# Kernel optimization log

Measured on AMD Instinct MI355X. Metric: run time of the kernel, lower is better.

Reference implementation:

```python
import jax, jax.numpy as jnp
import numpy as np

B = 16384          # batch
WIDTH = 128        # nodes per DAG layer
N_HIDDEN = 30      # hidden layers
DEG = 16           # in-degree of each non-source node
N_WL = N_HIDDEN + 1            # weighted layers (hidden + sink layer) = 31
N_NODES = (N_WL + 1) * WIDTH   # 32 layers * 128 = 4096 total DAG nodes


def setup_inputs() -> dict:
    rng = np.random.default_rng(0)
    # Mask M per layer: (preds+bias, layer_width); bias row (last) is all ones.
    masks = np.zeros((N_WL, WIDTH + 1, WIDTH), np.float32)
    masks[:, -1, :] = 1.0
    for l in range(N_WL):
        for j in range(WIDTH):
            rows = rng.choice(WIDTH, size=DEG, replace=False)
            masks[l, rows, j] = 1.0
    # kaiming_uniform_(a=sqrt(5)) on (nnz,1) tensors has fan_in=1 -> U(-1,1) per nnz entry.
    weights = (rng.uniform(-1.0, 1.0, masks.shape).astype(np.float32)) * masks
    # Layered DAG: preds of weighted layer l are exactly the nodes of layer l (global ids l*W..(l+1)*W).
    preds_idx = np.stack([np.arange(l * WIDTH, (l + 1) * WIDTH) for l in range(N_WL)]).astype(np.int32)
    layers_idx = preds_idx + WIDTH  # nodes written by weighted layer l
    x = jax.random.normal(jax.random.key(0), (B, WIDTH), jnp.float32)
    return {
        "x": x,
        "weights": jnp.asarray(weights),
        "masks": jnp.asarray(masks),
        "preds_idx": jnp.asarray(preds_idx),
        "layers_idx": jnp.asarray(layers_idx),
    }


def reference(x, weights, masks, preds_idx, layers_idx):
    b = x.shape[0]
    act = jnp.zeros((b, N_NODES), x.dtype)
    act = act.at[:, :WIDTH].set(x)           # activations[:, sources] = x
    ones = jnp.ones((b, 1), x.dtype)         # bias column (bias=True)
    # dropout p=0.0 -> identity

    def step(act, layer_inputs):
        W, M, preds, layer = layer_inputs
        h = jnp.concatenate([jnp.take(act, preds, axis=1), ones], axis=1)  # [b, preds+1]
        out = jax.nn.relu(h @ (M * W))                                     # [b, width]
        return act.at[:, layer].set(out), None

    act, _ = jax.lax.scan(step, act, (weights, masks, preds_idx, layers_idx))
    sinks = layers_idx[-1]
    return jnp.take(act, sinks, axis=1)       # activations[:, sinks]
```

## Files before the change

### kernel.cpp

```cpp
#include <hip/hip_runtime.h>
#include <stdint.h>

#define NWL 31

typedef __attribute__((ext_vector_type(8))) short short8;
typedef __attribute__((ext_vector_type(4))) float f32x4;
typedef __attribute__((ext_vector_type(4))) uint32_t u32x4;

#define WCOMP 32768
#define WLAYER 65536
#define WS_W_BYTES (NWL * WLAYER)

#define LDS_WBUF0 0
#define LDS_WBUF1 65536
#define LDS_ACT   131072
#define LDS_TOTAL 163840

__device__ __forceinline__ uint16_t f2bf(float f) {
  uint32_t u = __builtin_bit_cast(uint32_t, f);
  u += 0x7FFFu + ((u >> 16) & 1u);
  return (uint16_t)(u >> 16);
}
__device__ __forceinline__ float bf2f(uint16_t b) {
  return __builtin_bit_cast(float, (uint32_t)b << 16);
}

__device__ __forceinline__ uint32_t perm_hihi(uint32_t hi, uint32_t lo) {
#if __has_builtin(__builtin_amdgcn_perm)
  return __builtin_amdgcn_perm(hi, lo, 0x07060302u);
#else
  return (hi & 0xFFFF0000u) | (lo >> 16);
#endif
}
__device__ __forceinline__ uint32_t perm_lolo(uint32_t hi, uint32_t lo) {
#if __has_builtin(__builtin_amdgcn_perm)
  return __builtin_amdgcn_perm(hi, lo, 0x05040100u);
#else
  return (hi << 16) | (lo & 0xFFFFu);
#endif
}

__device__ __forceinline__ void gload_lds16(const void* g, void* l) {
  __builtin_amdgcn_global_load_lds(
      (const __attribute__((address_space(1))) uint32_t*)g,
      (__attribute__((address_space(3))) uint32_t*)l, 16, 0, 0);
}

__global__ __launch_bounds__(512)
void prep_weights(const float* __restrict__ W, const float* __restrict__ M,
                  char* __restrict__ wsW, float* __restrict__ wsB) {
  const int l    = blockIdx.x >> 2;
  const int kk   = blockIdx.x & 3;
  const int nt   = threadIdx.x >> 6;
  const int lane = threadIdx.x & 63;
  const int kbase = kk * 32 + ((lane >> 4) << 3);
  const int n     = (nt << 4) + (lane & 15);
  const float* Wl = W + l * 129 * 128;
  const float* Ml = M + l * 129 * 128;
  short8 vh, vl;
#pragma unroll
  for (int i = 0; i < 8; ++i) {
    const int k = kbase + i;
    const float v = Wl[k * 128 + n] * Ml[k * 128 + n];
    const uint16_t h = f2bf(v);
    vh[i] = (short)h;
    vl[i] = (short)f2bf(v - bf2f(h));
  }
  char* base = wsW + l * WLAYER;
  const int frag = ((kk * 8 + nt) * 64 + lane) * 16;
  *(short8*)(base + frag)         = vh;
  *(short8*)(base + WCOMP + frag) = vl;
  if (kk == 0 && threadIdx.x < 128) {
    const int t = threadIdx.x;
    wsB[l * 128 + t] = Wl[128 * 128 + t] * Ml[128 * 128 + t];
  }
}

__global__ __launch_bounds__(512, 2)
void dag_mlp(const float* __restrict__ x, const char* __restrict__ wsW,
             const float* __restrict__ wsB, float* __restrict__ out) {
  extern __shared__ char lds[];
  const int tid  = threadIdx.x;
  const int lane = tid & 63;
  const int wv   = tid >> 6;
  const int wm   = wv >> 2;
  const int wn   = wv & 3;
  const int l16  = lane & 15;
  const int g4   = lane >> 4;
  const int r0   = blockIdx.x << 6;

#pragma unroll
  for (int r = 0; r < 8; ++r) {
    const int off = r * 8192 + wv * 1024;
    gload_lds16(wsW + off + lane * 16, lds + LDS_WBUF0 + off);
  }

#pragma unroll
  for (int it = 0; it < 4; ++it) {
    const int idx = tid + it * 512;
    const int row = idx >> 5;
    const int cq  = idx & 31;
    const f32x4 v = *(const f32x4*)(x + (size_t)(r0 + row) * 128 + cq * 4);
    u32x4 w;
#pragma unroll
    for (int c = 0; c < 4; ++c) {
      const uint32_t u  = __builtin_bit_cast(uint32_t, v[c]);
      const float    hi = __builtin_bit_cast(float, u & 0xFFFF0000u);
      const uint32_t ur = __builtin_bit_cast(uint32_t, v[c] - hi);
      w[c] = perm_hihi(ur, u);
    }
    const int off = row * 512 + ((cq ^ (row & 7)) << 4);
    *(u32x4*)(lds + LDS_ACT + off) = w;
  }

  int aoff[2][4][2];
#pragma unroll
  for (int fr = 0; fr < 2; ++fr) {
    const int arow = wm * 32 + fr * 16 + l16;
#pragma unroll
    for (int kk = 0; kk < 4; ++kk) {
      const int g0 = kk * 8 + g4 * 2;
      aoff[fr][kk][0] = arow * 512 + (((g0    ) ^ (arow & 7)) << 4);
      aoff[fr][kk][1] = arow * 512 + (((g0 + 1) ^ (arow & 7)) << 4);
    }
  }
  int boff[4][2];
#pragma unroll
  for (int kk = 0; kk < 4; ++kk)
#pragma unroll
    for (int fc = 0; fc < 2; ++fc)
      boff[kk][fc] = (((kk * 8 + wn * 2 + fc) * 64 + lane) << 4);
  int eoff[2][2][4];
#pragma unroll
  for (int fr = 0; fr < 2; ++fr)
#pragma unroll
    for (int fc = 0; fc < 2; ++fc) {
      const int col = wn * 32 + fc * 16 + l16;
#pragma unroll
      for (int i = 0; i < 4; ++i) {
        const int row = wm * 32 + fr * 16 + g4 * 4 + i;
        eoff[fr][fc][i] = row * 512 + (((col >> 2) ^ (row & 7)) << 4) + ((col & 3) << 2);
      }
    }
  const float* biasp = wsB + wn * 32 + l16;

  __syncthreads();

  int wsel = 0;
  for (int l = 0; l < NWL; ++l) {
    if (l + 1 < NWL) {
      const char* g = wsW + (size_t)(l + 1) * WLAYER;
      const int dst = wsel ^ 65536;
#pragma unroll
      for (int r = 0; r < 8; ++r) {
        const int off = r * 8192 + wv * 1024;
        gload_lds16(g + off + lane * 16, lds + dst + off);
      }
    }
    const float bias0 = biasp[l * 128];
    const float bias1 = biasp[l * 128 + 16];

    u32x4 ah[2][4], al[2][4];
#pragma unroll
    for (int fr = 0; fr < 2; ++fr)
#pragma unroll
      for (int kk = 0; kk < 4; ++kk) {
        const u32x4 p0 = *(const u32x4*)(lds + LDS_ACT + aoff[fr][kk][0]);
        const u32x4 p1 = *(const u32x4*)(lds + LDS_ACT + aoff[fr][kk][1]);
        ah[fr][kk][0] = perm_lolo(p0[1], p0[0]);
        ah[fr][kk][1] = perm_lolo(p0[3], p0[2]);
        ah[fr][kk][2] = perm_lolo(p1[1], p1[0]);
        ah[fr][kk][3] = perm_lolo(p1[3], p1[2]);
        al[fr][kk][0] = perm_hihi(p0[1], p0[0]);
        al[fr][kk][1] = perm_hihi(p0[3], p0[2]);
        al[fr][kk][2] = perm_hihi(p1[1], p1[0]);
        al[fr][kk][3] = perm_hihi(p1[3], p1[2]);
      }

    f32x4 acc[2][2];
#pragma unroll
    for (int fr = 0; fr < 2; ++fr)
#pragma unroll
      for (int fc = 0; fc < 2; ++fc) {
        f32x4 z = {0.f, 0.f, 0.f, 0.f};
        acc[fr][fc] = z;
      }

#pragma unroll
    for (int kk = 0; kk < 4; ++kk) {
      short8 bH[2], bL[2];
#pragma unroll
      for (int fc = 0; fc < 2; ++fc) {
        const char* p = lds + wsel + boff[kk][fc];
        bH[fc] = *(const short8*)(p);
        bL[fc] = *(const short8*)(p + WCOMP);
      }
#pragma unroll
      for (int fr = 0; fr < 2; ++fr) {
        const short8 aH = __builtin_bit_cast(short8, ah[fr][kk]);
#pragma unroll
        for (int fc = 0; fc < 2; ++fc)
          acc[fr][fc] = __builtin_amdgcn_mfma_f32_16x16x32_bf16(aH, bH[fc], acc[fr][fc], 0, 0, 0);
      }
#pragma unroll
      for (int fr = 0; fr < 2; ++fr) {
        const short8 aL = __builtin_bit_cast(short8, al[fr][kk]);
#pragma unroll
        for (int fc = 0; fc < 2; ++fc)
          acc[fr][fc] = __builtin_amdgcn_mfma_f32_16x16x32_bf16(aL, bH[fc], acc[fr][fc], 0, 0, 0);
      }
#pragma unroll
      for (int fr = 0; fr < 2; ++fr) {
        const short8 aH = __builtin_bit_cast(short8, ah[fr][kk]);
#pragma unroll
        for (int fc = 0; fc < 2; ++fc)
          acc[fr][fc] = __builtin_amdgcn_mfma_f32_16x16x32_bf16(aH, bL[fc], acc[fr][fc], 0, 0, 0);
      }
    }

    __syncthreads();

    if (l == NWL - 1) {
#pragma unroll
      for (int fr = 0; fr < 2; ++fr)
#pragma unroll
        for (int fc = 0; fc < 2; ++fc) {
          const float bias = fc ? bias1 : bias0;
          const int col = wn * 32 + fc * 16 + l16;
#pragma unroll
          for (int i = 0; i < 4; ++i) {
            const int row = r0 + wm * 32 + fr * 16 + g4 * 4 + i;
            out[(size_t)row * 128 + col] = fmaxf(acc[fr][fc][i] + bias, 0.0f);
          }
        }
    } else {
#pragma unroll
      for (int fr = 0; fr < 2; ++fr)
#pragma unroll
        for (int fc = 0; fc < 2; ++fc) {
          const float bias = fc ? bias1 : bias0;
#pragma unroll
          for (int i = 0; i < 4; ++i) {
            const float v = fmaxf(acc[fr][fc][i] + bias, 0.0f);
            const uint32_t u  = __builtin_bit_cast(uint32_t, v);
            const float    hi = __builtin_bit_cast(float, u & 0xFFFF0000u);
            const uint32_t ur = __builtin_bit_cast(uint32_t, v - hi);
            *(uint32_t*)(lds + LDS_ACT + eoff[fr][fc][i]) = perm_hihi(ur, u);
          }
        }
      __syncthreads();
      wsel ^= 65536;
    }
  }
}

extern "C" void kernel_launch(void* const* d_in, const int* in_sizes, int n_in,
                              void* d_out, int out_size, void* d_ws, size_t ws_size,
                              hipStream_t stream) {
  const float* x = (const float*)d_in[0];
  const float* W = (const float*)d_in[1];
  const float* M = (const float*)d_in[2];
  char*  wsW = (char*)d_ws;
  float* wsB = (float*)((char*)d_ws + WS_W_BYTES);
  float* out = (float*)d_out;

  (void)hipFuncSetAttribute((const void*)dag_mlp,
                            hipFuncAttributeMaxDynamicSharedMemorySize, LDS_TOTAL);

  hipLaunchKernelGGL(prep_weights, dim3(NWL * 4), dim3(512), 0, stream, W, M, wsW, wsB);
  hipLaunchKernelGGL(dag_mlp, dim3(256), dim3(512), LDS_TOTAL, stream, x, wsW, wsB, out);
}
```

Measured before the change: 130.2 us.

## Load weight fragments directly into registers and double-buffer activations in LDS

Weight fragments are no longer staged through LDS with global_load_lds. Each wave now loads its own B fragments for the next layer straight from global memory (L2) into a register double buffer (B0/B1). Activations ping-pong between two LDS buffers, which leaves one barrier per layer instead of two and cuts LDS use from 160KB to 64KB. In exchange, register pressure goes up by 128 VGPRs for the weight buffers, and every wave refetches weights from global memory or cache instead of sharing one LDS copy.

```diff
diff --git a/kernel.cpp b/kernel.cpp
--- a/kernel.cpp
+++ b/kernel.cpp
@@ -11,10 +11,9 @@
 #define WLAYER 65536
 #define WS_W_BYTES (NWL * WLAYER)
 
-#define LDS_WBUF0 0
-#define LDS_WBUF1 65536
-#define LDS_ACT   131072
-#define LDS_TOTAL 163840
+#define LDS_ACT0 0
+#define LDS_ACT1 32768
+#define LDS_TOTAL 65536
 
 __device__ __forceinline__ uint16_t f2bf(float f) {
   uint32_t u = __builtin_bit_cast(uint32_t, f);
@@ -38,12 +37,6 @@
 #else
   return (hi << 16) | (lo & 0xFFFFu);
 #endif
-}
-
-__device__ __forceinline__ void gload_lds16(const void* g, void* l) {
-  __builtin_amdgcn_global_load_lds(
-      (const __attribute__((address_space(1))) uint32_t*)g,
-      (__attribute__((address_space(3))) uint32_t*)l, 16, 0, 0);
 }
 
 __global__ __launch_bounds__(512)
@@ -90,12 +83,6 @@
   const int r0   = blockIdx.x << 6;
 
 #pragma unroll
-  for (int r = 0; r < 8; ++r) {
-    const int off = r * 8192 + wv * 1024;
-    gload_lds16(wsW + off + lane * 16, lds + LDS_WBUF0 + off);
-  }
-
-#pragma unroll
   for (int it = 0; it < 4; ++it) {
     const int idx = tid + it * 512;
     const int row = idx >> 5;
@@ -110,7 +97,7 @@
       w[c] = perm_hihi(ur, u);
     }
     const int off = row * 512 + ((cq ^ (row & 7)) << 4);
-    *(u32x4*)(lds + LDS_ACT + off) = w;
+    *(u32x4*)(lds + LDS_ACT0 + off) = w;
   }
 
   int aoff[2][4][2];
@@ -124,12 +111,6 @@
       aoff[fr][kk][1] = arow * 512 + (((g0 + 1) ^ (arow & 7)) << 4);
     }
   }
-  int boff[4][2];
-#pragma unroll
-  for (int kk = 0; kk < 4; ++kk)
-#pragma unroll
-    for (int fc = 0; fc < 2; ++fc)
-      boff[kk][fc] = (((kk * 8 + wn * 2 + fc) * 64 + lane) << 4);
   int eoff[2][2][4];
 #pragma unroll
   for (int fr = 0; fr < 2; ++fr)
@@ -142,116 +123,109 @@
         eoff[fr][fc][i] = row * 512 + (((col >> 2) ^ (row & 7)) << 4) + ((col & 3) << 2);
       }
     }
-  const float* biasp = wsB + wn * 32 + l16;
+  const float* biasL = wsB + wn * 32 + l16;
+  const char*  wlane = wsW + wn * 2048 + (size_t)lane * 16;
+
+  u32x4 B0[16], B1[16];
+#pragma unroll
+  for (int kk = 0; kk < 4; ++kk)
+#pragma unroll
+    for (int fc = 0; fc < 2; ++fc)
+#pragma unroll
+      for (int hl = 0; hl < 2; ++hl)
+        B0[kk * 4 + fc * 2 + hl] =
+            *(const u32x4*)(wlane + kk * 8192 + fc * 1024 + hl * 32768);
 
   __syncthreads();
 
-  int wsel = 0;
-  for (int l = 0; l < NWL; ++l) {
-    if (l + 1 < NWL) {
-      const char* g = wsW + (size_t)(l + 1) * WLAYER;
-      const int dst = wsel ^ 65536;
-#pragma unroll
-      for (int r = 0; r < 8; ++r) {
-        const int off = r * 8192 + wv * 1024;
-        gload_lds16(g + off + lane * 16, lds + dst + off);
-      }
-    }
-    const float bias0 = biasp[l * 128];
-    const float bias1 = biasp[l * 128 + 16];
-
-    u32x4 ah[2][4], al[2][4];
-#pragma unroll
-    for (int fr = 0; fr < 2; ++fr)
-#pragma unroll
-      for (int kk = 0; kk < 4; ++kk) {
-        const u32x4 p0 = *(const u32x4*)(lds + LDS_ACT + aoff[fr][kk][0]);
-        const u32x4 p1 = *(const u32x4*)(lds + LDS_ACT + aoff[fr][kk][1]);
-        ah[fr][kk][0] = perm_lolo(p0[1], p0[0]);
-        ah[fr][kk][1] = perm_lolo(p0[3], p0[2]);
-        ah[fr][kk][2] = perm_lolo(p1[1], p1[0]);
-        ah[fr][kk][3] = perm_lolo(p1[3], p1[2]);
-        al[fr][kk][0] = perm_hihi(p0[1], p0[0]);
-        al[fr][kk][1] = perm_hihi(p0[3], p0[2]);
-        al[fr][kk][2] = perm_hihi(p1[1], p1[0]);
-        al[fr][kk][3] = perm_hihi(p1[3], p1[2]);
-      }
-
-    f32x4 acc[2][2];
-#pragma unroll
-    for (int fr = 0; fr < 2; ++fr)
-#pragma unroll
-      for (int fc = 0; fc < 2; ++fc) {
-        f32x4 z = {0.f, 0.f, 0.f, 0.f};
-        acc[fr][fc] = z;
-      }
-
-#pragma unroll
-    for (int kk = 0; kk < 4; ++kk) {
-      short8 bH[2], bL[2];
-#pragma unroll
-      for (int fc = 0; fc < 2; ++fc) {
-        const char* p = lds + wsel + boff[kk][fc];
-        bH[fc] = *(const short8*)(p);
-        bL[fc] = *(const short8*)(p + WCOMP);
-      }
-#pragma unroll
-      for (int fr = 0; fr < 2; ++fr) {
-        const short8 aH = __builtin_bit_cast(short8, ah[fr][kk]);
-#pragma unroll
-        for (int fc = 0; fc < 2; ++fc)
-          acc[fr][fc] = __builtin_amdgcn_mfma_f32_16x16x32_bf16(aH, bH[fc], acc[fr][fc], 0, 0, 0);
-      }
-#pragma unroll
-      for (int fr = 0; fr < 2; ++fr) {
-        const short8 aL = __builtin_bit_cast(short8, al[fr][kk]);
-#pragma unroll
-        for (int fc = 0; fc < 2; ++fc)
-          acc[fr][fc] = __builtin_amdgcn_mfma_f32_16x16x32_bf16(aL, bH[fc], acc[fr][fc], 0, 0, 0);
-      }
-#pragma unroll
-      for (int fr = 0; fr < 2; ++fr) {
-        const short8 aH = __builtin_bit_cast(short8, ah[fr][kk]);
-#pragma unroll
-        for (int fc = 0; fc < 2; ++fc)
-          acc[fr][fc] = __builtin_amdgcn_mfma_f32_16x16x32_bf16(aH, bL[fc], acc[fr][fc], 0, 0, 0);
-      }
-    }
-
-    __syncthreads();
-
-    if (l == NWL - 1) {
-#pragma unroll
-      for (int fr = 0; fr < 2; ++fr)
-#pragma unroll
-        for (int fc = 0; fc < 2; ++fc) {
-          const float bias = fc ? bias1 : bias0;
-          const int col = wn * 32 + fc * 16 + l16;
-#pragma unroll
-          for (int i = 0; i < 4; ++i) {
-            const int row = r0 + wm * 32 + fr * 16 + g4 * 4 + i;
-            out[(size_t)row * 128 + col] = fmaxf(acc[fr][fc][i] + bias, 0.0f);
-          }
-        }
-    } else {
-#pragma unroll
-      for (int fr = 0; fr < 2; ++fr)
-#pragma unroll
-        for (int fc = 0; fc < 2; ++fc) {
-          const float bias = fc ? bias1 : bias0;
-#pragma unroll
-          for (int i = 0; i < 4; ++i) {
-            const float v = fmaxf(acc[fr][fc][i] + bias, 0.0f);
-            const uint32_t u  = __builtin_bit_cast(uint32_t, v);
-            const float    hi = __builtin_bit_cast(float, u & 0xFFFF0000u);
-            const uint32_t ur = __builtin_bit_cast(uint32_t, v - hi);
-            *(uint32_t*)(lds + LDS_ACT + eoff[fr][fc][i]) = perm_hihi(ur, u);
-          }
-        }
-      __syncthreads();
-      wsel ^= 65536;
-    }
-  }
+#define LAYER_BODY(l, Bc, Bn, RDB, WRB, LAST, PREF)                            \
+  do {                                                                         \
+    if (PREF) {                                                                \
+      const char* wl = wlane + (size_t)((l) + 1) * WLAYER;                     \
+      _Pragma("unroll") for (int kk = 0; kk < 4; ++kk)                         \
+      _Pragma("unroll") for (int fc = 0; fc < 2; ++fc)                         \
+      _Pragma("unroll") for (int hl = 0; hl < 2; ++hl)                         \
+        (Bn)[kk * 4 + fc * 2 + hl] =                                           \
+            *(const u32x4*)(wl + kk * 8192 + fc * 1024 + hl * 32768);          \
+    }                                                                          \
+    const float bias0 = biasL[(l) * 128];                                      \
+    const float bias1 = biasL[(l) * 128 + 16];                                 \
+    f32x4 acc[2][2];                                                           \
+    _Pragma("unroll") for (int fr = 0; fr < 2; ++fr)                           \
+    _Pragma("unroll") for (int fc = 0; fc < 2; ++fc) {                         \
+      f32x4 z = {0.f, 0.f, 0.f, 0.f};                                          \
+      acc[fr][fc] = z;                                                         \
+    }                                                                          \
+    _Pragma("unroll") for (int kk = 0; kk < 4; ++kk) {                         \
+      const u32x4 p00 = *(const u32x4*)(lds + (RDB) + aoff[0][kk][0]);         \
+      const u32x4 p01 = *(const u32x4*)(lds + (RDB) + aoff[0][kk][1]);         \
+      const u32x4 p10 = *(const u32x4*)(lds + (RDB) + aoff[1][kk][0]);         \
+      const u32x4 p11 = *(const u32x4*)(lds + (RDB) + aoff[1][kk][1]);         \
+      u32x4 h0, l0, h1, l1;                                                    \
+      h0[0] = perm_lolo(p00[1], p00[0]);  h0[1] = perm_lolo(p00[3], p00[2]);   \
+      h0[2] = perm_lolo(p01[1], p01[0]);  h0[3] = perm_lolo(p01[3], p01[2]);   \
+      l0[0] = perm_hihi(p00[1], p00[0]);  l0[1] = perm_hihi(p00[3], p00[2]);   \
+      l0[2] = perm_hihi(p01[1], p01[0]);  l0[3] = perm_hihi(p01[3], p01[2]);   \
+      h1[0] = perm_lolo(p10[1], p10[0]);  h1[1] = perm_lolo(p10[3], p10[2]);   \
+      h1[2] = perm_lolo(p11[1], p11[0]);  h1[3] = perm_lolo(p11[3], p11[2]);   \
+      l1[0] = perm_hihi(p10[1], p10[0]);  l1[1] = perm_hihi(p10[3], p10[2]);   \
+      l1[2] = perm_hihi(p11[1], p11[0]);  l1[3] = perm_hihi(p11[3], p11[2]);   \
+      const short8 a0H = __builtin_bit_cast(short8, h0);                       \
+      const short8 a0L = __builtin_bit_cast(short8, l0);                       \
+      const short8 a1H = __builtin_bit_cast(short8, h1);                       \
+      const short8 a1L = __builtin_bit_cast(short8, l1);                       \
+      const short8 bH0 = __builtin_bit_cast(short8, (Bc)[kk * 4 + 0]);         \
+      const short8 bL0 = __builtin_bit_cast(short8, (Bc)[kk * 4 + 1]);         \
+      const short8 bH1 = __builtin_bit_cast(short8, (Bc)[kk * 4 + 2]);         \
+      const short8 bL1 = __builtin_bit_cast(short8, (Bc)[kk * 4 + 3]);         \
+      acc[0][0] = __builtin_amdgcn_mfma_f32_16x16x32_bf16(a0H, bH0, acc[0][0], 0, 0, 0); \
+      acc[0][1] = __builtin_amdgcn_mfma_f32_16x16x32_bf16(a0H, bH1, acc[0][1], 0, 0, 0); \
+      acc[1][0] = __builtin_amdgcn_mfma_f32_16x16x32_bf16(a1H, bH0, acc[1][0], 0, 0, 0); \
+      acc[1][1] = __builtin_amdgcn_mfma_f32_16x16x32_bf16(a1H, bH1, acc[1][1], 0, 0, 0); \
+      acc[0][0] = __builtin_amdgcn_mfma_f32_16x16x32_bf16(a0L, bH0, acc[0][0], 0, 0, 0); \
+      acc[0][1] = __builtin_amdgcn_mfma_f32_16x16x32_bf16(a0L, bH1, acc[0][1], 0, 0, 0); \
+      acc[1][0] = __builtin_amdgcn_mfma_f32_16x16x32_bf16(a1L, bH0, acc[1][0], 0, 0, 0); \
+      acc[1][1] = __builtin_amdgcn_mfma_f32_16x16x32_bf16(a1L, bH1, acc[1][1], 0, 0, 0); \
+      acc[0][0] = __builtin_amdgcn_mfma_f32_16x16x32_bf16(a0H, bL0, acc[0][0], 0, 0, 0); \
+      acc[0][1] = __builtin_amdgcn_mfma_f32_16x16x32_bf16(a0H, bL1, acc[0][1], 0, 0, 0); \
+      acc[1][0] = __builtin_amdgcn_mfma_f32_16x16x32_bf16(a1H, bL0, acc[1][0], 0, 0, 0); \
+      acc[1][1] = __builtin_amdgcn_mfma_f32_16x16x32_bf16(a1H, bL1, acc[1][1], 0, 0, 0); \
+    }                                                                          \
+    if (LAST) {                                                                \
+      _Pragma("unroll") for (int fr = 0; fr < 2; ++fr)                         \
+      _Pragma("unroll") for (int fc = 0; fc < 2; ++fc) {                       \
+        const float bias = fc ? bias1 : bias0;                                 \
+        const int col = wn * 32 + fc * 16 + l16;                               \
+        _Pragma("unroll") for (int i = 0; i < 4; ++i) {                        \
+          const int row = r0 + wm * 32 + fr * 16 + g4 * 4 + i;                 \
+          out[(size_t)row * 128 + col] = fmaxf(acc[fr][fc][i] + bias, 0.0f);   \
+        }                                                                      \
+      }                                                                        \
+    } else {                                                                   \
+      _Pragma("unroll") for (int fr = 0; fr < 2; ++fr)                         \
+      _Pragma("unroll") for (int fc = 0; fc < 2; ++fc) {                       \
+        const float bias = fc ? bias1 : bias0;                                 \
+        _Pragma("unroll") for (int i = 0; i < 4; ++i) {                        \
+          const float v = fmaxf(acc[fr][fc][i] + bias, 0.0f);                  \
+          const uint32_t u  = __builtin_bit_cast(uint32_t, v);                 \
+          const float    hi = __builtin_bit_cast(float, u & 0xFFFF0000u);      \
+          const uint32_t ur = __builtin_bit_cast(uint32_t, v - hi);            \
+          *(uint32_t*)(lds + (WRB) + eoff[fr][fc][i]) = perm_hihi(ur, u);      \
+        }                                                                      \
+      }                                                                        \
+    }                                                                          \
+    __syncthreads();                                                           \
+  } while (0)
+
+  for (int lp = 0; lp < 16; ++lp) {
+    const int l0 = 2 * lp;
+    LAYER_BODY(l0, B0, B1, LDS_ACT0, LDS_ACT1, l0 == NWL - 1, l0 + 1 < NWL);
+    if (l0 + 1 < NWL) {
+      const int l1 = l0 + 1;
+      LAYER_BODY(l1, B1, B0, LDS_ACT1, LDS_ACT0, false, l1 + 1 < NWL);
+    }
+  }
+#undef LAYER_BODY
 }
 
 extern "C" void kernel_launch(void* const* d_in, const int* in_sizes, int n_in,
```

After: 124.6 us. 4.3% less time.

## Load weights directly into registers and double-buffer activations in LDS

Applied to the files above, without the earlier changes.

Drops the LDS double-buffered weight staging. Each wave now loads its own B fragments (hi and lo bf16) straight from global memory into registers, prefetching the next layer's fragments after the current MFMAs. Activations are ping-ponged between two LDS buffers, which removes one __syncthreads per layer. LDS use falls to 64KB and launch bounds rise to 4 blocks per CU, trading extra VGPR pressure and global/L2 traffic for higher occupancy and fewer barriers.

```diff
diff --git a/kernel.cpp b/kernel.cpp
--- a/kernel.cpp
+++ b/kernel.cpp
@@ -11,10 +11,9 @@
 #define WLAYER 65536
 #define WS_W_BYTES (NWL * WLAYER)
 
-#define LDS_WBUF0 0
-#define LDS_WBUF1 65536
-#define LDS_ACT   131072
-#define LDS_TOTAL 163840
+#define LDS_ACT0 0
+#define LDS_ACT1 32768
+#define LDS_TOTAL 65536
 
 __device__ __forceinline__ uint16_t f2bf(float f) {
   uint32_t u = __builtin_bit_cast(uint32_t, f);
@@ -38,12 +37,6 @@
 #else
   return (hi << 16) | (lo & 0xFFFFu);
 #endif
-}
-
-__device__ __forceinline__ void gload_lds16(const void* g, void* l) {
-  __builtin_amdgcn_global_load_lds(
-      (const __attribute__((address_space(1))) uint32_t*)g,
-      (__attribute__((address_space(3))) uint32_t*)l, 16, 0, 0);
 }
 
 __global__ __launch_bounds__(512)
@@ -76,7 +69,7 @@
   }
 }
 
-__global__ __launch_bounds__(512, 2)
+__global__ __launch_bounds__(512, 4)
 void dag_mlp(const float* __restrict__ x, const char* __restrict__ wsW,
              const float* __restrict__ wsB, float* __restrict__ out) {
   extern __shared__ char lds[];
@@ -90,12 +83,6 @@
   const int r0   = blockIdx.x << 6;
 
 #pragma unroll
-  for (int r = 0; r < 8; ++r) {
-    const int off = r * 8192 + wv * 1024;
-    gload_lds16(wsW + off + lane * 16, lds + LDS_WBUF0 + off);
-  }
-
-#pragma unroll
   for (int it = 0; it < 4; ++it) {
     const int idx = tid + it * 512;
     const int row = idx >> 5;
@@ -110,73 +97,48 @@
       w[c] = perm_hihi(ur, u);
     }
     const int off = row * 512 + ((cq ^ (row & 7)) << 4);
-    *(u32x4*)(lds + LDS_ACT + off) = w;
-  }
-
-  int aoff[2][4][2];
+    *(u32x4*)(lds + LDS_ACT0 + off) = w;
+  }
+
+  int aAddr[2][2];
 #pragma unroll
   for (int fr = 0; fr < 2; ++fr) {
     const int arow = wm * 32 + fr * 16 + l16;
 #pragma unroll
-    for (int kk = 0; kk < 4; ++kk) {
-      const int g0 = kk * 8 + g4 * 2;
-      aoff[fr][kk][0] = arow * 512 + (((g0    ) ^ (arow & 7)) << 4);
-      aoff[fr][kk][1] = arow * 512 + (((g0 + 1) ^ (arow & 7)) << 4);
-    }
-  }
-  int boff[4][2];
+    for (int b = 0; b < 2; ++b)
+      aAddr[fr][b] = LDS_ACT0 + arow * 512 + (((g4 * 2 + b) ^ (arow & 7)) << 4);
+  }
+  int eBase[2][2], eD[4];
+#pragma unroll
+  for (int fr = 0; fr < 2; ++fr) {
+    const int R0 = wm * 32 + fr * 16 + g4 * 4;
+#pragma unroll
+    for (int fc = 0; fc < 2; ++fc)
+      eBase[fr][fc] = LDS_ACT1 + R0 * 512 + wn * 128 +
+                      ((fc ^ (g4 & 1)) << 6) + ((l16 & 3) << 2);
+  }
+#pragma unroll
+  for (int i = 0; i < 4; ++i)
+    eD[i] = i * 512 + (((l16 >> 2) ^ i) << 4);
+
+  const float* biasLp = wsB + wn * 32 + l16;
+  const char*  wlane  = wsW + wn * 2048 + (size_t)lane * 16;
+
+  u32x4 Bc[16];
 #pragma unroll
   for (int kk = 0; kk < 4; ++kk)
 #pragma unroll
     for (int fc = 0; fc < 2; ++fc)
-      boff[kk][fc] = (((kk * 8 + wn * 2 + fc) * 64 + lane) << 4);
-  int eoff[2][2][4];
-#pragma unroll
-  for (int fr = 0; fr < 2; ++fr)
-#pragma unroll
-    for (int fc = 0; fc < 2; ++fc) {
-      const int col = wn * 32 + fc * 16 + l16;
-#pragma unroll
-      for (int i = 0; i < 4; ++i) {
-        const int row = wm * 32 + fr * 16 + g4 * 4 + i;
-        eoff[fr][fc][i] = row * 512 + (((col >> 2) ^ (row & 7)) << 4) + ((col & 3) << 2);
-      }
-    }
-  const float* biasp = wsB + wn * 32 + l16;
+#pragma unroll
+      for (int hl = 0; hl < 2; ++hl)
+        Bc[kk * 4 + fc * 2 + hl] =
+            *(const u32x4*)(wlane + kk * 8192 + fc * 1024 + hl * 32768);
 
   __syncthreads();
 
-  int wsel = 0;
   for (int l = 0; l < NWL; ++l) {
-    if (l + 1 < NWL) {
-      const char* g = wsW + (size_t)(l + 1) * WLAYER;
-      const int dst = wsel ^ 65536;
-#pragma unroll
-      for (int r = 0; r < 8; ++r) {
-        const int off = r * 8192 + wv * 1024;
-        gload_lds16(g + off + lane * 16, lds + dst + off);
-      }
-    }
-    const float bias0 = biasp[l * 128];
-    const float bias1 = biasp[l * 128 + 16];
-
-    u32x4 ah[2][4], al[2][4];
-#pragma unroll
-    for (int fr = 0; fr < 2; ++fr)
-#pragma unroll
-      for (int kk = 0; kk < 4; ++kk) {
-        const u32x4 p0 = *(const u32x4*)(lds + LDS_ACT + aoff[fr][kk][0]);
-        const u32x4 p1 = *(const u32x4*)(lds + LDS_ACT + aoff[fr][kk][1]);
-        ah[fr][kk][0] = perm_lolo(p0[1], p0[0]);
-        ah[fr][kk][1] = perm_lolo(p0[3], p0[2]);
-        ah[fr][kk][2] = perm_lolo(p1[1], p1[0]);
-        ah[fr][kk][3] = perm_lolo(p1[3], p1[2]);
-        al[fr][kk][0] = perm_hihi(p0[1], p0[0]);
-        al[fr][kk][1] = perm_hihi(p0[3], p0[2]);
-        al[fr][kk][2] = perm_hihi(p1[1], p1[0]);
-        al[fr][kk][3] = perm_hihi(p1[3], p1[2]);
-      }
-
+    const float bias0 = biasLp[l * 128];
+    const float bias1 = biasLp[l * 128 + 16];
     f32x4 acc[2][2];
 #pragma unroll
     for (int fr = 0; fr < 2; ++fr)
@@ -188,37 +150,41 @@
 
 #pragma unroll
     for (int kk = 0; kk < 4; ++kk) {
-      short8 bH[2], bL[2];
-#pragma unroll
-      for (int fc = 0; fc < 2; ++fc) {
-        const char* p = lds + wsel + boff[kk][fc];
-        bH[fc] = *(const short8*)(p);
-        bL[fc] = *(const short8*)(p + WCOMP);
+      const short8 bH0 = __builtin_bit_cast(short8, Bc[kk * 4 + 0]);
+      const short8 bL0 = __builtin_bit_cast(short8, Bc[kk * 4 + 1]);
+      const short8 bH1 = __builtin_bit_cast(short8, Bc[kk * 4 + 2]);
+      const short8 bL1 = __builtin_bit_cast(short8, Bc[kk * 4 + 3]);
+#pragma unroll
+      for (int fr = 0; fr < 2; ++fr) {
+        const u32x4 p0 = *(const u32x4*)(lds + aAddr[fr][0] + kk * 128);
+        const u32x4 p1 = *(const u32x4*)(lds + aAddr[fr][1] + kk * 128);
+        u32x4 hh, llv;
+        hh[0]  = perm_lolo(p0[1], p0[0]);  hh[1]  = perm_lolo(p0[3], p0[2]);
+        hh[2]  = perm_lolo(p1[1], p1[0]);  hh[3]  = perm_lolo(p1[3], p1[2]);
+        llv[0] = perm_hihi(p0[1], p0[0]);  llv[1] = perm_hihi(p0[3], p0[2]);
+        llv[2] = perm_hihi(p1[1], p1[0]);  llv[3] = perm_hihi(p1[3], p1[2]);
+        const short8 aH = __builtin_bit_cast(short8, hh);
+        const short8 aL = __builtin_bit_cast(short8, llv);
+        acc[fr][0] = __builtin_amdgcn_mfma_f32_16x16x32_bf16(aH, bH0, acc[fr][0], 0, 0, 0);
+        acc[fr][1] = __builtin_amdgcn_mfma_f32_16x16x32_bf16(aH, bH1, acc[fr][1], 0, 0, 0);
+        acc[fr][0] = __builtin_amdgcn_mfma_f32_16x16x32_bf16(aL, bH0, acc[fr][0], 0, 0, 0);
+        acc[fr][1] = __builtin_amdgcn_mfma_f32_16x16x32_bf16(aL, bH1, acc[fr][1], 0, 0, 0);
+        acc[fr][0] = __builtin_amdgcn_mfma_f32_16x16x32_bf16(aH, bL0, acc[fr][0], 0, 0, 0);
+        acc[fr][1] = __builtin_amdgcn_mfma_f32_16x16x32_bf16(aH, bL1, acc[fr][1], 0, 0, 0);
       }
-#pragma unroll
-      for (int fr = 0; fr < 2; ++fr) {
-        const short8 aH = __builtin_bit_cast(short8, ah[fr][kk]);
+    }
+
+    if (l + 1 < NWL) {
+      const char* wl = wlane + (size_t)(l + 1) * WLAYER;
+#pragma unroll
+      for (int kk = 0; kk < 4; ++kk)
 #pragma unroll
         for (int fc = 0; fc < 2; ++fc)
-          acc[fr][fc] = __builtin_amdgcn_mfma_f32_16x16x32_bf16(aH, bH[fc], acc[fr][fc], 0, 0, 0);
-      }
-#pragma unroll
-      for (int fr = 0; fr < 2; ++fr) {
-        const short8 aL = __builtin_bit_cast(short8, al[fr][kk]);
-#pragma unroll
-        for (int fc = 0; fc < 2; ++fc)
-          acc[fr][fc] = __builtin_amdgcn_mfma_f32_16x16x32_bf16(aL, bH[fc], acc[fr][fc], 0, 0, 0);
-      }
-#pragma unroll
-      for (int fr = 0; fr < 2; ++fr) {
-        const short8 aH = __builtin_bit_cast(short8, ah[fr][kk]);
-#pragma unroll
-        for (int fc = 0; fc < 2; ++fc)
-          acc[fr][fc] = __builtin_amdgcn_mfma_f32_16x16x32_bf16(aH, bL[fc], acc[fr][fc], 0, 0, 0);
-      }
-    }
-
-    __syncthreads();
+#pragma unroll
+          for (int hl = 0; hl < 2; ++hl)
+            Bc[kk * 4 + fc * 2 + hl] =
+                *(const u32x4*)(wl + kk * 8192 + fc * 1024 + hl * 32768);
+    }
 
     if (l == NWL - 1) {
 #pragma unroll
@@ -245,12 +211,16 @@
             const uint32_t u  = __builtin_bit_cast(uint32_t, v);
             const float    hi = __builtin_bit_cast(float, u & 0xFFFF0000u);
             const uint32_t ur = __builtin_bit_cast(uint32_t, v - hi);
-            *(uint32_t*)(lds + LDS_ACT + eoff[fr][fc][i]) = perm_hihi(ur, u);
+            *(uint32_t*)(lds + eBase[fr][fc] + eD[i]) = perm_hihi(ur, u);
           }
         }
-      __syncthreads();
-      wsel ^= 65536;
-    }
+#pragma unroll
+      for (int fr = 0; fr < 2; ++fr) {
+        aAddr[fr][0] ^= 32768; aAddr[fr][1] ^= 32768;
+        eBase[fr][0] ^= 32768; eBase[fr][1] ^= 32768;
+      }
+    }
+    __syncthreads();
   }
 }
 
```

After: 141.1 us. 8.4% more time.
